# Optimization experiments

Hardware: AMD Instinct MI355X
Metric: run time of the kernel (lower is better)

The kernel has to match this reference:

```python
import jax, jax.numpy as jnp
import numpy as np

EMBED_DIM = 64
HIDDEN_DIM = 320
CONTEXT_DIM = 768

def setup_inputs() -> dict:
    key = jax.random.key(0)
    k1, k2, k3, k4, k5 = jax.random.split(key, 5)
    B, T, S = 4, 4096, 4096
    tokens = jax.random.normal(k1, (B, T, HIDDEN_DIM), dtype=jnp.float32)
    context = jax.random.normal(k2, (B, S, CONTEXT_DIM), dtype=jnp.float32)
    # nn.Linear(in, out, bias=False) weights, stored as [out, in] like torch
    sq = 1.0 / np.sqrt(HIDDEN_DIM)
    sk = 1.0 / np.sqrt(CONTEXT_DIM)
    Wq = jax.random.uniform(k3, (EMBED_DIM, HIDDEN_DIM), minval=-sq, maxval=sq, dtype=jnp.float32)
    Wk = jax.random.uniform(k4, (EMBED_DIM, CONTEXT_DIM), minval=-sk, maxval=sk, dtype=jnp.float32)
    Wv = jax.random.uniform(k5, (HIDDEN_DIM, CONTEXT_DIM), minval=-sk, maxval=sk, dtype=jnp.float32)
    return {"tokens": tokens, "context": context, "Wq": Wq, "Wk": Wk, "Wv": Wv}

def reference(tokens, context, Wq, Wk, Wv):
    # Q: [B,T,E], K: [B,S,E], V: [B,S,Hd]
    Q = jnp.einsum('bth,eh->bte', tokens, Wq)
    K = jnp.einsum('bsc,ec->bse', context, Wk)
    V = jnp.einsum('bsc,hc->bsh', context, Wv)
    scores = jnp.einsum('bte,bse->bts', Q, K) / np.sqrt(EMBED_DIM)
    attn = jax.nn.softmax(scores, axis=-1)  # [B,T,S] full score matrix as in original
    ctx_vecs = jnp.einsum('bts,bsh->bth', attn, V)
    return ctx_vecs
```

## Files before the change

kernel.cpp:

```cpp
#include <hip/hip_runtime.h>
#include <hip/hip_bf16.h>

typedef _Float16 half4_t  __attribute__((ext_vector_type(4)));
typedef _Float16 half8_t  __attribute__((ext_vector_type(8)));
typedef float    float4_t __attribute__((ext_vector_type(4)));

#define MFMA16x32(a, b, c) __builtin_amdgcn_mfma_f32_16x16x32_f16(a, b, c, 0, 0, 0)

template <int KTOT, int NT, int MODE>
__device__ __forceinline__ void proj_body(const float* __restrict__ A,
                                          const float* __restrict__ W,
                                          _Float16* __restrict__ out, float sc,
                                          int m0, int n0, int htg0,
                                          _Float16* Ach, _Float16* Bch) {
  constexpr int NCH = KTOT / 64;
  constexpr int NTIL = NT / 16;
  const int tid = threadIdx.x, w = tid >> 6, lane = tid & 63;
  const int G = lane >> 4, l15 = lane & 15;

  float4_t acc[NTIL];
#pragma unroll
  for (int nt = 0; nt < NTIL; ++nt) acc[nt] = {0.f, 0.f, 0.f, 0.f};

  float4_t areg[4], wreg[NTIL];
  auto ldA = [&](int kc) {
#pragma unroll
    for (int t = 0; t < 4; ++t) {
      int idx = t * 256 + tid;
      areg[t] = *(const float4_t*)(A + (size_t)(m0 + (idx >> 4)) * KTOT + kc * 64 + (idx & 15) * 4);
    }
  };
  auto ldW = [&](int kc) {
#pragma unroll
    for (int t = 0; t < NTIL; ++t) {
      int idx = t * 256 + tid;
      wreg[t] = *(const float4_t*)(W + (size_t)(n0 + (idx >> 4)) * KTOT + kc * 64 + (idx & 15) * 4);
    }
  };

  ldA(0); ldW(0);
  for (int kc = 0; kc < NCH; ++kc) {
    __syncthreads();
#pragma unroll
    for (int t = 0; t < 4; ++t) {
      int idx = t * 256 + tid;
      half4_t h = {(_Float16)areg[t][0], (_Float16)areg[t][1], (_Float16)areg[t][2], (_Float16)areg[t][3]};
      *(half4_t*)(Ach + (idx >> 4) * 72 + (idx & 15) * 4) = h;
    }
#pragma unroll
    for (int t = 0; t < NTIL; ++t) {
      int idx = t * 256 + tid;
      half4_t h = {(_Float16)wreg[t][0], (_Float16)wreg[t][1], (_Float16)wreg[t][2], (_Float16)wreg[t][3]};
      *(half4_t*)(Bch + (idx >> 4) * 72 + (idx & 15) * 4) = h;
    }
    __syncthreads();
    if (kc + 1 < NCH) { ldA(kc + 1); ldW(kc + 1); }
#pragma unroll
    for (int c = 0; c < 2; ++c) {
      half8_t af = *(const half8_t*)(Ach + (w * 16 + l15) * 72 + c * 32 + 8 * G);
#pragma unroll
      for (int nt = 0; nt < NTIL; ++nt) {
        half8_t bf = *(const half8_t*)(Bch + (nt * 16 + l15) * 72 + c * 32 + 8 * G);
        acc[nt] = MFMA16x32(af, bf, acc[nt]);
      }
    }
  }

  if constexpr (MODE <= 1) {
#pragma unroll
    for (int nt = 0; nt < NTIL; ++nt)
#pragma unroll
      for (int r = 0; r < 4; ++r)
        out[(size_t)(m0 + w * 16 + 4 * G + r) * 64 + nt * 16 + l15] = (_Float16)(acc[nt][r] * sc);
  } else {
    __syncthreads();
#pragma unroll
    for (int nt = 0; nt < NTIL; ++nt) {
      half4_t h = {(_Float16)acc[nt][0], (_Float16)acc[nt][1], (_Float16)acc[nt][2], (_Float16)acc[nt][3]};
      *(half4_t*)(Bch + (nt * 16 + l15) * 72 + w * 16 + 4 * G) = h;
    }
    __syncthreads();
#pragma unroll
    for (int rep = 0; rep < 5; ++rep) {
      int idx = w * 5 + rep;
      int c2 = idx / 10, htl = idx % 10;
      half8_t fr = *(const half8_t*)(Bch + (htl * 16 + l15) * 72 + c2 * 32 + 8 * G);
      int sg = m0 + c2 * 32;
      int b = sg >> 12, c2b = (sg & 4095) >> 5;
      int htg = htg0 + htl;
      *(half8_t*)(out + ((size_t)((b * 128 + c2b) * 20 + htg)) * 512 + lane * 8) = fr;
    }
  }
}

__global__ __launch_bounds__(256, 2)
void qkv_proj_kernel(const float* __restrict__ tokens, const float* __restrict__ context,
                     const float* __restrict__ Wq, const float* __restrict__ Wk,
                     const float* __restrict__ Wv, _Float16* __restrict__ Q,
                     _Float16* __restrict__ K, _Float16* __restrict__ V) {
  __shared__ alignas(16) _Float16 smem[16128];
  _Float16* Ach = smem;
  _Float16* Bch = smem + 64 * 72;
  const int bx = blockIdx.x;
  const float qsc = 0.125f * 1.44269504088896f;
  if (bx < 512) {
    int y = bx >> 8, mb = bx & 255;
    proj_body<768, 160, 2>(context, Wv, V, 1.0f, mb * 64, y * 160, y * 10, Ach, Bch);
  } else if (bx < 768) {
    proj_body<768, 64, 1>(context, Wk, K, 1.0f, (bx - 512) * 64, 0, 0, Ach, Bch);
  } else {
    proj_body<320, 64, 0>(tokens, Wq, Q, qsc, (bx - 768) * 64, 0, 0, Ach, Bch);
  }
}

__global__ __launch_bounds__(512, 1)
void flash_kernel(const _Float16* __restrict__ Qg, const _Float16* __restrict__ Kg,
                  const _Float16* __restrict__ Vt, float* __restrict__ out) {
  __shared__ alignas(16) _Float16 kbuf[2][2048];
  __shared__ alignas(16) _Float16 pbuf[2][2048];
  __shared__ float larr[2][4][16];
  __shared__ float linv[64];

  const int tid = threadIdx.x, w = tid >> 6, lane = tid & 63;
  const int G = lane >> 4, l15 = lane & 15;
  const int bx = blockIdx.x;
  const int b = (bx & 7) >> 1;
  const int tblk = ((bx & 1) * 32 + (bx >> 3)) * 64;

  const bool is_pv = (w < 4);
  const int sw = w & 3;
  const int stile = sw & 1, tthalf = sw >> 1;
  const int t2 = tid & 255;
  const int s_loc = t2 >> 3, e8 = t2 & 7;
  const int kdst = ((s_loc >> 4) * 2 + (e8 >> 2)) * 512 + ((e8 & 3) * 16 + (s_loc & 15)) * 8;
  const _Float16* kg = Kg + (size_t)(b * 4096) * 64 + s_loc * 64 + e8 * 8;
  const _Float16* vt_b = Vt + (size_t)b * 1310720;

  half8_t qf[2][2];
  float la[2] = {0.f, 0.f};
  float4_t oa[4][5];
#pragma unroll
  for (int tt = 0; tt < 4; ++tt)
#pragma unroll
    for (int ht = 0; ht < 5; ++ht) oa[tt][ht] = {0.f, 0.f, 0.f, 0.f};
  half8_t vb[2][5];

  auto st_step = [&](int j) {
    half8_t af[2];
#pragma unroll
    for (int c = 0; c < 2; ++c)
      af[c] = *(const half8_t*)(&kbuf[j & 1][(stile * 2 + c) * 512 + lane * 8]);
#pragma unroll
    for (int tt2 = 0; tt2 < 2; ++tt2) {
      float4_t sa = {0.f, 0.f, 0.f, 0.f};
#pragma unroll
      for (int c = 0; c < 2; ++c) sa = MFMA16x32(af[c], qf[tt2][c], sa);
      float e0 = exp2f(sa[0]), e1 = exp2f(sa[1]), e2 = exp2f(sa[2]), e3 = exp2f(sa[3]);
      la[tt2] += (e0 + e1) + (e2 + e3);
      int tt = tthalf * 2 + tt2;
      int Gp = stile * 2 + (G >> 1);
      half4_t p = {(_Float16)e0, (_Float16)e1, (_Float16)e2, (_Float16)e3};
      *(half4_t*)(&pbuf[j & 1][tt * 512 + (Gp * 16 + l15) * 8 + 4 * (G & 1)]) = p;
    }
  };

  if (!is_pv) {
    uint4 k0 = *(const uint4*)(kg);
    uint4 k1 = *(const uint4*)(kg + 2048);
    *(uint4*)(&kbuf[0][kdst]) = k0;
    *(uint4*)(&kbuf[1][kdst]) = k1;
#pragma unroll
    for (int tt2 = 0; tt2 < 2; ++tt2) {
      int tt = tthalf * 2 + tt2;
#pragma unroll
      for (int c = 0; c < 2; ++c)
        qf[tt2][c] = *(const half8_t*)(Qg + (size_t)(b * 4096 + tblk + tt * 16 + l15) * 64 + c * 32 + 8 * G);
    }
  } else {
#pragma unroll
    for (int ht = 0; ht < 5; ++ht)
      vb[0][ht] = *(const half8_t*)(vt_b + (w * 5 + ht) * 512 + lane * 8);
  }
  __syncthreads();

  if (!is_pv) st_step(0);
  __syncthreads();

  for (int ii = 0; ii < 128; ii += 2) {
#pragma unroll
    for (int u = 0; u < 2; ++u) {
      const int i = ii + u;
      if (is_pv) {
        if (i < 127) {
#pragma unroll
          for (int ht = 0; ht < 5; ++ht)
            vb[u ^ 1][ht] = *(const half8_t*)(vt_b + (size_t)(i + 1) * 10240 + (w * 5 + ht) * 512 + lane * 8);
        }
        half8_t pa[4];
#pragma unroll
        for (int tt = 0; tt < 4; ++tt)
          pa[tt] = *(const half8_t*)(&pbuf[i & 1][tt * 512 + lane * 8]);
#pragma unroll
        for (int ht = 0; ht < 5; ++ht)
#pragma unroll
          for (int tt = 0; tt < 4; ++tt) oa[tt][ht] = MFMA16x32(pa[tt], vb[u][ht], oa[tt][ht]);
      } else {
        uint4 kreg;
        if (i < 126) kreg = *(const uint4*)(kg + (size_t)(i + 2) * 2048);
        if (i < 127) st_step(i + 1);
        if (i < 126) *(uint4*)(&kbuf[i & 1][kdst]) = kreg;
      }
      asm volatile("s_waitcnt lgkmcnt(0)" ::: "memory");
      __builtin_amdgcn_s_barrier();
    }
  }

  if (!is_pv) {
#pragma unroll
    for (int tt2 = 0; tt2 < 2; ++tt2) {
      float v = la[tt2];
      v += __shfl_xor(v, 16);
      v += __shfl_xor(v, 32);
      if (lane < 16) larr[stile][tthalf * 2 + tt2][l15] = v;
    }
  }
  __syncthreads();
  if (tid < 64) linv[tid] = 1.0f / (larr[0][tid >> 4][tid & 15] + larr[1][tid >> 4][tid & 15]);
  __syncthreads();
  if (is_pv) {
#pragma unroll
    for (int tt = 0; tt < 4; ++tt)
#pragma unroll
      for (int r = 0; r < 4; ++r) {
        float inv = linv[tt * 16 + 4 * G + r];
        size_t row = (size_t)(b * 4096 + tblk + tt * 16 + 4 * G + r) * 320;
#pragma unroll
        for (int ht = 0; ht < 5; ++ht)
          out[row + w * 80 + ht * 16 + l15] = oa[tt][ht][r] * inv;
      }
  }
}

extern "C" void kernel_launch(void* const* d_in, const int* in_sizes, int n_in,
                              void* d_out, int out_size, void* d_ws, size_t ws_size,
                              hipStream_t stream) {
  const float* tokens  = (const float*)d_in[0];
  const float* context = (const float*)d_in[1];
  const float* Wq      = (const float*)d_in[2];
  const float* Wk      = (const float*)d_in[3];
  const float* Wv      = (const float*)d_in[4];

  _Float16* Qws = (_Float16*)d_ws;
  _Float16* Kws = Qws + (size_t)1048576;
  _Float16* Vws = Kws + (size_t)1048576;

  qkv_proj_kernel<<<dim3(1024), 256, 0, stream>>>(tokens, context, Wq, Wk, Wv,
                                                  Qws, Kws, Vws);
  flash_kernel<<<dim3(256), 512, 0, stream>>>(Qws, Kws, Vws, (float*)d_out);
}
```

Measured before the change: 208.2 us.

## Double the per-iteration key chunk and halve flash loop barriers

The attention loop now processes 64 keys per iteration instead of 32. Each of the four score waves owns a 16-key slice across all four query tiles, and the PV waves consume two key chunks per step, so there are half as many block-wide barriers. Shared K and P buffers double, V prefetch registers double, and launch bounds ask for 2 blocks per CU. The cost is higher register and LDS pressure and a longer critical path per step.

```diff
diff --git a/kernel.cpp b/kernel.cpp
--- a/kernel.cpp
+++ b/kernel.cpp
@@ -113,12 +113,12 @@
   }
 }
 
-__global__ __launch_bounds__(512, 1)
+__global__ __launch_bounds__(512, 2)
 void flash_kernel(const _Float16* __restrict__ Qg, const _Float16* __restrict__ Kg,
                   const _Float16* __restrict__ Vt, float* __restrict__ out) {
-  __shared__ alignas(16) _Float16 kbuf[2][2048];
-  __shared__ alignas(16) _Float16 pbuf[2][2048];
-  __shared__ float larr[2][4][16];
+  __shared__ alignas(16) _Float16 kbuf[2][4096];
+  __shared__ alignas(16) _Float16 pbuf[2][4096];
+  __shared__ float larr[4][4][16];
   __shared__ float linv[64];
 
   const int tid = threadIdx.x, w = tid >> 6, lane = tid & 63;
@@ -128,104 +128,122 @@
   const int tblk = ((bx & 1) * 32 + (bx >> 3)) * 64;
 
   const bool is_pv = (w < 4);
-  const int sw = w & 3;
-  const int stile = sw & 1, tthalf = sw >> 1;
+  const int sw = w - 4;
   const int t2 = tid & 255;
   const int s_loc = t2 >> 3, e8 = t2 & 7;
   const int kdst = ((s_loc >> 4) * 2 + (e8 >> 2)) * 512 + ((e8 & 3) * 16 + (s_loc & 15)) * 8;
   const _Float16* kg = Kg + (size_t)(b * 4096) * 64 + s_loc * 64 + e8 * 8;
   const _Float16* vt_b = Vt + (size_t)b * 1310720;
 
-  half8_t qf[2][2];
-  float la[2] = {0.f, 0.f};
+  half8_t qf[4][2];
+  float la[4] = {0.f, 0.f, 0.f, 0.f};
   float4_t oa[4][5];
 #pragma unroll
   for (int tt = 0; tt < 4; ++tt)
 #pragma unroll
     for (int ht = 0; ht < 5; ++ht) oa[tt][ht] = {0.f, 0.f, 0.f, 0.f};
-  half8_t vb[2][5];
+  half8_t vb[2][2][5];
 
   auto st_step = [&](int j) {
     half8_t af[2];
 #pragma unroll
     for (int c = 0; c < 2; ++c)
-      af[c] = *(const half8_t*)(&kbuf[j & 1][(stile * 2 + c) * 512 + lane * 8]);
-#pragma unroll
-    for (int tt2 = 0; tt2 < 2; ++tt2) {
+      af[c] = *(const half8_t*)(&kbuf[j & 1][(sw * 2 + c) * 512 + lane * 8]);
+    const int pbase = ((l15 + 16 * ((sw & 1) * 2 + (G >> 1)))) * 8 + 4 * (G & 1);
+#pragma unroll
+    for (int tt = 0; tt < 4; ++tt) {
       float4_t sa = {0.f, 0.f, 0.f, 0.f};
-#pragma unroll
-      for (int c = 0; c < 2; ++c) sa = MFMA16x32(af[c], qf[tt2][c], sa);
+      sa = MFMA16x32(af[0], qf[tt][0], sa);
+      sa = MFMA16x32(af[1], qf[tt][1], sa);
       float e0 = exp2f(sa[0]), e1 = exp2f(sa[1]), e2 = exp2f(sa[2]), e3 = exp2f(sa[3]);
-      la[tt2] += (e0 + e1) + (e2 + e3);
-      int tt = tthalf * 2 + tt2;
-      int Gp = stile * 2 + (G >> 1);
+      la[tt] += (e0 + e1) + (e2 + e3);
       half4_t p = {(_Float16)e0, (_Float16)e1, (_Float16)e2, (_Float16)e3};
-      *(half4_t*)(&pbuf[j & 1][tt * 512 + (Gp * 16 + l15) * 8 + 4 * (G & 1)]) = p;
+      *(half4_t*)(&pbuf[j & 1][(tt * 2 + (sw >> 1)) * 512 + pbase]) = p;
     }
   };
 
   if (!is_pv) {
-    uint4 k0 = *(const uint4*)(kg);
-    uint4 k1 = *(const uint4*)(kg + 2048);
-    *(uint4*)(&kbuf[0][kdst]) = k0;
-    *(uint4*)(&kbuf[1][kdst]) = k1;
-#pragma unroll
-    for (int tt2 = 0; tt2 < 2; ++tt2) {
-      int tt = tthalf * 2 + tt2;
+    uint4 k00 = *(const uint4*)(kg);
+    uint4 k01 = *(const uint4*)(kg + 2048);
+    uint4 k10 = *(const uint4*)(kg + 4096);
+    uint4 k11 = *(const uint4*)(kg + 4096 + 2048);
+    *(uint4*)(&kbuf[0][kdst]) = k00;
+    *(uint4*)(&kbuf[0][kdst + 2048]) = k01;
+    *(uint4*)(&kbuf[1][kdst]) = k10;
+    *(uint4*)(&kbuf[1][kdst + 2048]) = k11;
+#pragma unroll
+    for (int tt = 0; tt < 4; ++tt)
 #pragma unroll
       for (int c = 0; c < 2; ++c)
-        qf[tt2][c] = *(const half8_t*)(Qg + (size_t)(b * 4096 + tblk + tt * 16 + l15) * 64 + c * 32 + 8 * G);
-    }
+        qf[tt][c] = *(const half8_t*)(Qg + (size_t)(b * 4096 + tblk + tt * 16 + l15) * 64 + c * 32 + 8 * G);
+  }
+  __syncthreads();
+
+  if (is_pv) {
+#pragma unroll
+    for (int sc = 0; sc < 2; ++sc)
+#pragma unroll
+      for (int ht = 0; ht < 5; ++ht)
+        vb[0][sc][ht] = *(const half8_t*)(vt_b + (size_t)sc * 10240 + (w * 5 + ht) * 512 + lane * 8);
   } else {
-#pragma unroll
-    for (int ht = 0; ht < 5; ++ht)
-      vb[0][ht] = *(const half8_t*)(vt_b + (w * 5 + ht) * 512 + lane * 8);
-  }
-  __syncthreads();
-
-  if (!is_pv) st_step(0);
-  __syncthreads();
-
-  for (int ii = 0; ii < 128; ii += 2) {
+    st_step(0);
+  }
+  __syncthreads();
+
+  for (int ii = 0; ii < 64; ii += 2) {
 #pragma unroll
     for (int u = 0; u < 2; ++u) {
       const int i = ii + u;
       if (is_pv) {
-        if (i < 127) {
+        if (i < 63) {
+#pragma unroll
+          for (int sc = 0; sc < 2; ++sc)
+#pragma unroll
+            for (int ht = 0; ht < 5; ++ht)
+              vb[u ^ 1][sc][ht] = *(const half8_t*)(vt_b + (size_t)(2 * (i + 1) + sc) * 10240 + (w * 5 + ht) * 512 + lane * 8);
+        }
+        half8_t pa[4][2];
+#pragma unroll
+        for (int tt = 0; tt < 4; ++tt)
+#pragma unroll
+          for (int sc = 0; sc < 2; ++sc)
+            pa[tt][sc] = *(const half8_t*)(&pbuf[i & 1][(tt * 2 + sc) * 512 + lane * 8]);
+#pragma unroll
+        for (int sc = 0; sc < 2; ++sc)
 #pragma unroll
           for (int ht = 0; ht < 5; ++ht)
-            vb[u ^ 1][ht] = *(const half8_t*)(vt_b + (size_t)(i + 1) * 10240 + (w * 5 + ht) * 512 + lane * 8);
+#pragma unroll
+            for (int tt = 0; tt < 4; ++tt)
+              oa[tt][ht] = MFMA16x32(pa[tt][sc], vb[u][sc][ht], oa[tt][ht]);
+      } else {
+        uint4 kr0, kr1;
+        if (i < 62) {
+          kr0 = *(const uint4*)(kg + (size_t)(i + 2) * 4096);
+          kr1 = *(const uint4*)(kg + (size_t)(i + 2) * 4096 + 2048);
         }
-        half8_t pa[4];
-#pragma unroll
-        for (int tt = 0; tt < 4; ++tt)
-          pa[tt] = *(const half8_t*)(&pbuf[i & 1][tt * 512 + lane * 8]);
-#pragma unroll
-        for (int ht = 0; ht < 5; ++ht)
-#pragma unroll
-          for (int tt = 0; tt < 4; ++tt) oa[tt][ht] = MFMA16x32(pa[tt], vb[u][ht], oa[tt][ht]);
-      } else {
-        uint4 kreg;
-        if (i < 126) kreg = *(const uint4*)(kg + (size_t)(i + 2) * 2048);
-        if (i < 127) st_step(i + 1);
-        if (i < 126) *(uint4*)(&kbuf[i & 1][kdst]) = kreg;
+        if (i < 63) st_step(i + 1);
+        if (i < 62) {
+          *(uint4*)(&kbuf[i & 1][kdst]) = kr0;
+          *(uint4*)(&kbuf[i & 1][kdst + 2048]) = kr1;
+        }
       }
-      asm volatile("s_waitcnt lgkmcnt(0)" ::: "memory");
-      __builtin_amdgcn_s_barrier();
+      __syncthreads();
     }
   }
 
   if (!is_pv) {
 #pragma unroll
-    for (int tt2 = 0; tt2 < 2; ++tt2) {
-      float v = la[tt2];
+    for (int tt = 0; tt < 4; ++tt) {
+      float v = la[tt];
       v += __shfl_xor(v, 16);
       v += __shfl_xor(v, 32);
-      if (lane < 16) larr[stile][tthalf * 2 + tt2][l15] = v;
-    }
-  }
-  __syncthreads();
-  if (tid < 64) linv[tid] = 1.0f / (larr[0][tid >> 4][tid & 15] + larr[1][tid >> 4][tid & 15]);
+      if (lane < 16) larr[sw][tt][l15] = v;
+    }
+  }
+  __syncthreads();
+  if (tid < 64)
+    linv[tid] = 1.0f / (larr[0][tid >> 4][tid & 15] + larr[1][tid >> 4][tid & 15] +
+                        larr[2][tid >> 4][tid & 15] + larr[3][tid >> 4][tid & 15]);
   __syncthreads();
   if (is_pv) {
 #pragma unroll
```

After: 196.9 us. 1.06x faster.
